# Performance work log

Measured on AMD Instinct MI355X. Metric: run time of the kernel, lower is better.

Reference implementation:

```python
import jax, jax.numpy as jnp
import numpy as np

B, T, L = 512, 512, 128  # batch, seq_len, tag-vocab size (incl. START=126, STOP=127)


def setup_inputs() -> dict:
    key = jax.random.key(0)
    k1, k2, k3 = jax.random.split(key, 3)
    # scale emissions so exp(gold path score) stays finite in fp32
    feats = jax.random.normal(k1, (B, T, L), dtype=jnp.float32) * 0.05
    # xavier_normal on [L, L] -> std = sqrt(2/(L+L)) = 1/sqrt(L)
    transfer = jax.random.normal(k2, (L, L), dtype=jnp.float32) * (1.0 / np.sqrt(L))
    target = jax.random.randint(k3, (B, T), 0, L - 2, dtype=jnp.int32)
    return {"feats": feats, "transfer": transfer, "target": target,
            "start": L - 2, "stop": L - 1}


def _crf_loss(feats, transfer, target, start, stop):
    # feats: [B, T, L] emissions; transfer: [L, L]; target: [B, T] gold tags
    Bb, Tt, Ll = feats.shape

    # ---- forward algorithm (log-sum-exp DP over tags) ----
    # scores[1] = feats[1] + transfer[start, :]
    prev0 = feats[:, 1] + transfer[start][None, :]  # [B, L]

    def step(prev, f_t):
        # original: scores[t, y] = LSE_x( scores[t-1, x] + feats[t, x] + transfer[x, y] )
        v = prev + f_t                                        # [B, L] over prev-tag x
        new = jax.nn.logsumexp(v[:, :, None] + transfer[None, :, :], axis=1)  # [B, L]
        return new, None

    step = jax.checkpoint(step)  # keep scan residuals to just the carries
    feats_rest = jnp.swapaxes(feats[:, 2:], 0, 1)  # [T-2, B, L]
    prev, _ = jax.lax.scan(step, prev0, feats_rest)
    sentence_score = jax.nn.logsumexp(prev + transfer[:, stop][None, :], axis=1)  # [B]

    # ---- gold path score ----
    emit0 = feats[:, 0, start]  # hh[0, start]
    emit = jnp.take_along_axis(feats[:, 1:], target[:, 1:, None], axis=2)[..., 0].sum(axis=1)
    pre = jnp.concatenate(
        [jnp.full((Bb, 1), start, dtype=target.dtype), target[:, 1:Tt - 1]], axis=1)  # [B, T-1]
    # original reads transfer[pre, tgt].data[0] -> detached constant
    trans = jax.lax.stop_gradient(transfer[pre, target[:, 1:]]).sum(axis=1)
    gold_score = jnp.exp(emit0 + emit + trans)  # original returns torch.exp(score)

    return sentence_score - gold_score  # per-sentence loss, shape [B]


def reference(feats, transfer, target, start, stop):
    return _crf_loss(feats, transfer, target, start, stop)
```

## Files before the change

### kernel.cpp

```cpp
#include <hip/hip_runtime.h>
#include <hip/hip_bf16.h>

#define T_DIM 512
#define L_DIM 128

typedef _Float16 h2 __attribute__((ext_vector_type(2)));

#if defined(__has_builtin)
#if __has_builtin(__builtin_amdgcn_fdot2)
#define HAS_FDOT2 1
#endif
#endif

__device__ __forceinline__ float fdot2_acc(h2 a, h2 b, float c) {
#ifdef HAS_FDOT2
    return __builtin_amdgcn_fdot2(a, b, c, false);
#else
    return c + (float)a.x * (float)b.x + (float)a.y * (float)b.y;
#endif
}

__device__ __forceinline__ h2 pack_f16(float a, float b) {
    return __builtin_bit_cast(h2, __builtin_amdgcn_cvt_pkrtz(a, b));
}

__device__ __forceinline__ void lds_barrier() {
    asm volatile("s_waitcnt lgkmcnt(0)\n\ts_barrier" ::: "memory");
}

__global__ __launch_bounds__(512, 4) void crf_fwd_kernel(
    const float* __restrict__ feats,
    const float* __restrict__ transfer,
    const int* __restrict__ target,
    const int* __restrict__ startp,
    const int* __restrict__ stopp,
    float* __restrict__ out)
{
    __shared__ unsigned short LdsU[2][L_DIM] __attribute__((aligned(16)));
    __shared__ float LdsRed[32];

    const int tid  = threadIdx.x;
    const int lane = tid & 63;
    const int wv   = tid >> 6;
    const int jj   = lane & 15;
    const int iq   = lane >> 4;
    const int j    = (wv << 4) | jj;
    const int i0   = iq << 5;
    const int b    = blockIdx.x;
    const int start = startp[0];
    const int stop  = stopp[0];
    const float* fbase = feats + (size_t)b * T_DIM * L_DIM;
    const float LOG128 = 4.852030263919617f;

    h2 Ecol[16];
#pragma unroll
    for (int q = 0; q < 16; ++q) {
        float e0 = __expf(transfer[(i0 + 2 * q)     * L_DIM + j]) * 0.0078125f;
        float e1 = __expf(transfer[(i0 + 2 * q + 1) * L_DIM + j]) * 0.0078125f;
        Ecol[q] = pack_f16(e0, e1);
    }
    const float trStop = transfer[j * L_DIM + stop];

    {
        float v2 = fbase[1 * L_DIM + j] + fbase[2 * L_DIM + j]
                 + transfer[start * L_DIM + j];
        if (iq == 0) {
            _Float16 h = (_Float16)__expf(v2);
            LdsU[0][j] = __builtin_bit_cast(unsigned short, h);
        }
    }
    float fa = fbase[3 * L_DIM + j];
    float fb = fbase[4 * L_DIM + j];
    float S  = 0.f;
    lds_barrier();

    int cur = 0;
    float accFinal = 0.f;

    for (int t = 2; t <= T_DIM - 1; ++t) {
        int tp = t + 3; if (tp > T_DIM - 1) tp = T_DIM - 1;
        float fnew = fbase[tp * L_DIM + j];
        float fexp = __expf(fa);

        if ((t & 15) == 0) {
            _Float16 h0 = __builtin_bit_cast(_Float16, LdsU[cur][0]);
            float u0 = (float)h0;
            fexp *= 1.0f / u0;
            S += __logf(u0);
        }

        const uint4* P4 = reinterpret_cast<const uint4*>(&LdsU[cur][0]);
        uint4 pa = P4[(iq << 2) | 0];
        uint4 pb = P4[(iq << 2) | 1];
        uint4 pc = P4[(iq << 2) | 2];
        uint4 pd = P4[(iq << 2) | 3];

        float a0 = 0.f, a1 = 0.f, a2 = 0.f, a3 = 0.f;
        a0 = fdot2_acc(__builtin_bit_cast(h2, pa.x), Ecol[0],  a0);
        a0 = fdot2_acc(__builtin_bit_cast(h2, pa.y), Ecol[1],  a0);
        a0 = fdot2_acc(__builtin_bit_cast(h2, pa.z), Ecol[2],  a0);
        a0 = fdot2_acc(__builtin_bit_cast(h2, pa.w), Ecol[3],  a0);
        a1 = fdot2_acc(__builtin_bit_cast(h2, pb.x), Ecol[4],  a1);
        a1 = fdot2_acc(__builtin_bit_cast(h2, pb.y), Ecol[5],  a1);
        a1 = fdot2_acc(__builtin_bit_cast(h2, pb.z), Ecol[6],  a1);
        a1 = fdot2_acc(__builtin_bit_cast(h2, pb.w), Ecol[7],  a1);
        a2 = fdot2_acc(__builtin_bit_cast(h2, pc.x), Ecol[8],  a2);
        a2 = fdot2_acc(__builtin_bit_cast(h2, pc.y), Ecol[9],  a2);
        a2 = fdot2_acc(__builtin_bit_cast(h2, pc.z), Ecol[10], a2);
        a2 = fdot2_acc(__builtin_bit_cast(h2, pc.w), Ecol[11], a2);
        a3 = fdot2_acc(__builtin_bit_cast(h2, pd.x), Ecol[12], a3);
        a3 = fdot2_acc(__builtin_bit_cast(h2, pd.y), Ecol[13], a3);
        a3 = fdot2_acc(__builtin_bit_cast(h2, pd.z), Ecol[14], a3);
        a3 = fdot2_acc(__builtin_bit_cast(h2, pd.w), Ecol[15], a3);
        float acc = (a0 + a1) + (a2 + a3);

        acc += __shfl_xor(acc, 16);
        acc += __shfl_xor(acc, 32);

        if (t < T_DIM - 1) {
            float un = acc * fexp;
            fa = fb; fb = fnew;
            if (iq == 0) {
                _Float16 h = (_Float16)un;
                LdsU[cur ^ 1][j] = __builtin_bit_cast(unsigned short, h);
            }
            lds_barrier();
            cur ^= 1;
        } else {
            accFinal = acc;
        }
    }

    S += 510.0f * LOG128;

    float x  = __logf(accFinal) + S + trStop;
    float mx = x;
#pragma unroll
    for (int d = 1; d < 64; d <<= 1) mx = fmaxf(mx, __shfl_xor(mx, d));
    float ex = (iq == 0) ? __expf(x - mx) : 0.f;
#pragma unroll
    for (int d = 1; d < 64; d <<= 1) ex += __shfl_xor(ex, d);
    if (lane == 0) { LdsRed[wv] = mx; LdsRed[8 + wv] = ex; }

    float es = 0.f, ts = 0.f;
    {
        int t = 1 + tid;
        if (t < T_DIM) {
            int tg = target[b * T_DIM + t];
            es = fbase[t * L_DIM + tg];
            int pr = (t == 1) ? start : target[b * T_DIM + t - 1];
            ts = transfer[pr * L_DIM + tg];
        }
    }
#pragma unroll
    for (int d = 1; d < 64; d <<= 1) {
        es += __shfl_xor(es, d);
        ts += __shfl_xor(ts, d);
    }
    if (lane == 0) { LdsRed[16 + wv] = es; LdsRed[24 + wv] = ts; }
    __syncthreads();

    if (tid == 0) {
        float M = LdsRed[0];
#pragma unroll
        for (int k = 1; k < 8; ++k) M = fmaxf(M, LdsRed[k]);
        float Ssum = 0.f;
#pragma unroll
        for (int k = 0; k < 8; ++k) Ssum += LdsRed[8 + k] * __expf(LdsRed[k] - M);
        float sentence = M + __logf(Ssum);
        float em = 0.f, tn = 0.f;
#pragma unroll
        for (int k = 0; k < 8; ++k) { em += LdsRed[16 + k]; tn += LdsRed[24 + k]; }
        float emit0 = fbase[start];
        out[b] = sentence - __expf(emit0 + em + tn);
    }
}

extern "C" void kernel_launch(void* const* d_in, const int* in_sizes, int n_in,
                              void* d_out, int out_size, void* d_ws, size_t ws_size,
                              hipStream_t stream) {
    const float* feats    = (const float*)d_in[0];
    const float* transfer = (const float*)d_in[1];
    const int*   target   = (const int*)d_in[2];
    const int*   startp   = (const int*)d_in[3];
    const int*   stopp    = (const int*)d_in[4];
    float* outp = (float*)d_out;
    int B = in_sizes[0] / (T_DIM * L_DIM);
    hipLaunchKernelGGL(crf_fwd_kernel, dim3(B), dim3(512), 0, stream,
                       feats, transfer, target, startp, stopp, outp);
}
```

Measured before the change: 395.1 us.

## Map each sequence to a single wavefront to eliminate block barriers

Reassigns each sentence's forward recursion to one 64-lane wavefront, with each lane computing two target tags against all 128 previous tags from register-resident exp(transfer) in half precision. Workgroup barriers and cross-lane shuffle reductions per timestep are removed, relying on single-wave execution with only an LDS waitcnt. This trades the serial synchronisation cost for eight times more dot-product work per lane per step and much lower occupancy. Final reductions also collapse to wave-level shuffles.

```diff
diff --git a/kernel.cpp b/kernel.cpp
--- a/kernel.cpp
+++ b/kernel.cpp
@@ -1,10 +1,10 @@
 #include <hip/hip_runtime.h>
-#include <hip/hip_bf16.h>
 
 #define T_DIM 512
 #define L_DIM 128
 
 typedef _Float16 h2 __attribute__((ext_vector_type(2)));
+typedef float f2 __attribute__((ext_vector_type(2)));
 
 #if defined(__has_builtin)
 #if __has_builtin(__builtin_amdgcn_fdot2)
@@ -20,15 +20,15 @@
 #endif
 }
 
-__device__ __forceinline__ h2 pack_f16(float a, float b) {
+__device__ __forceinline__ unsigned int pack_u32(float a, float b) {
+    return __builtin_bit_cast(unsigned int, __builtin_amdgcn_cvt_pkrtz(a, b));
+}
+
+__device__ __forceinline__ h2 pack_h2(float a, float b) {
     return __builtin_bit_cast(h2, __builtin_amdgcn_cvt_pkrtz(a, b));
 }
 
-__device__ __forceinline__ void lds_barrier() {
-    asm volatile("s_waitcnt lgkmcnt(0)\n\ts_barrier" ::: "memory");
-}
-
-__global__ __launch_bounds__(512, 4) void crf_fwd_kernel(
+__global__ __launch_bounds__(64, 1) void crf_fwd_kernel(
     const float* __restrict__ feats,
     const float* __restrict__ transfer,
     const int* __restrict__ target,
@@ -36,120 +36,110 @@
     const int* __restrict__ stopp,
     float* __restrict__ out)
 {
-    __shared__ unsigned short LdsU[2][L_DIM] __attribute__((aligned(16)));
-    __shared__ float LdsRed[32];
+    __shared__ unsigned int LdsU[2][64] __attribute__((aligned(16)));
 
-    const int tid  = threadIdx.x;
-    const int lane = tid & 63;
-    const int wv   = tid >> 6;
-    const int jj   = lane & 15;
-    const int iq   = lane >> 4;
-    const int j    = (wv << 4) | jj;
-    const int i0   = iq << 5;
+    const int lane = threadIdx.x;
+    const int j0   = lane << 1;
     const int b    = blockIdx.x;
     const int start = startp[0];
     const int stop  = stopp[0];
     const float* fbase = feats + (size_t)b * T_DIM * L_DIM;
     const float LOG128 = 4.852030263919617f;
+    const float SCALE  = 0.0078125f;
 
-    h2 Ecol[16];
+    h2 E0[64], E1[64];
 #pragma unroll
-    for (int q = 0; q < 16; ++q) {
-        float e0 = __expf(transfer[(i0 + 2 * q)     * L_DIM + j]) * 0.0078125f;
-        float e1 = __expf(transfer[(i0 + 2 * q + 1) * L_DIM + j]) * 0.0078125f;
-        Ecol[q] = pack_f16(e0, e1);
+    for (int q = 0; q < 64; ++q) {
+        f2 r0 = *reinterpret_cast<const f2*>(&transfer[(2 * q)     * L_DIM + j0]);
+        f2 r1 = *reinterpret_cast<const f2*>(&transfer[(2 * q + 1) * L_DIM + j0]);
+        E0[q] = pack_h2(__expf(r0.x) * SCALE, __expf(r1.x) * SCALE);
+        E1[q] = pack_h2(__expf(r0.y) * SCALE, __expf(r1.y) * SCALE);
     }
-    const float trStop = transfer[j * L_DIM + stop];
+    const float trStop0 = transfer[j0 * L_DIM + stop];
+    const float trStop1 = transfer[(j0 + 1) * L_DIM + stop];
 
     {
-        float v2 = fbase[1 * L_DIM + j] + fbase[2 * L_DIM + j]
-                 + transfer[start * L_DIM + j];
-        if (iq == 0) {
-            _Float16 h = (_Float16)__expf(v2);
-            LdsU[0][j] = __builtin_bit_cast(unsigned short, h);
-        }
+        f2 f1v = *reinterpret_cast<const f2*>(&fbase[1 * L_DIM + j0]);
+        f2 f2v = *reinterpret_cast<const f2*>(&fbase[2 * L_DIM + j0]);
+        f2 tsv = *reinterpret_cast<const f2*>(&transfer[start * L_DIM + j0]);
+        float v0 = f1v.x + f2v.x + tsv.x;
+        float v1 = f1v.y + f2v.y + tsv.y;
+        LdsU[0][lane] = pack_u32(__expf(v0), __expf(v1));
     }
-    float fa = fbase[3 * L_DIM + j];
-    float fb = fbase[4 * L_DIM + j];
-    float S  = 0.f;
-    lds_barrier();
+    f2 fa2 = *reinterpret_cast<const f2*>(&fbase[3 * L_DIM + j0]);
+    f2 fb2 = *reinterpret_cast<const f2*>(&fbase[4 * L_DIM + j0]);
+    f2 fc2 = *reinterpret_cast<const f2*>(&fbase[5 * L_DIM + j0]);
+    float S = 0.f;
+    asm volatile("s_waitcnt lgkmcnt(0)" ::: "memory");
 
     int cur = 0;
-    float accFinal = 0.f;
+    float accF0 = 0.f, accF1 = 0.f;
 
     for (int t = 2; t <= T_DIM - 1; ++t) {
-        int tp = t + 3; if (tp > T_DIM - 1) tp = T_DIM - 1;
-        float fnew = fbase[tp * L_DIM + j];
-        float fexp = __expf(fa);
+        int tp = t + 4; if (tp > T_DIM - 1) tp = T_DIM - 1;
+        f2 fnew2 = *reinterpret_cast<const f2*>(&fbase[tp * L_DIM + j0]);
+        float e0 = __expf(fa2.x);
+        float e1 = __expf(fa2.y);
 
         if ((t & 15) == 0) {
-            _Float16 h0 = __builtin_bit_cast(_Float16, LdsU[cur][0]);
-            float u0 = (float)h0;
-            fexp *= 1.0f / u0;
+            h2 h = __builtin_bit_cast(h2, LdsU[cur][0]);
+            float u0 = (float)h.x;
+            float r = 1.0f / u0;
+            e0 *= r; e1 *= r;
             S += __logf(u0);
         }
 
-        const uint4* P4 = reinterpret_cast<const uint4*>(&LdsU[cur][0]);
-        uint4 pa = P4[(iq << 2) | 0];
-        uint4 pb = P4[(iq << 2) | 1];
-        uint4 pc = P4[(iq << 2) | 2];
-        uint4 pd = P4[(iq << 2) | 3];
-
-        float a0 = 0.f, a1 = 0.f, a2 = 0.f, a3 = 0.f;
-        a0 = fdot2_acc(__builtin_bit_cast(h2, pa.x), Ecol[0],  a0);
-        a0 = fdot2_acc(__builtin_bit_cast(h2, pa.y), Ecol[1],  a0);
-        a0 = fdot2_acc(__builtin_bit_cast(h2, pa.z), Ecol[2],  a0);
-        a0 = fdot2_acc(__builtin_bit_cast(h2, pa.w), Ecol[3],  a0);
-        a1 = fdot2_acc(__builtin_bit_cast(h2, pb.x), Ecol[4],  a1);
-        a1 = fdot2_acc(__builtin_bit_cast(h2, pb.y), Ecol[5],  a1);
-        a1 = fdot2_acc(__builtin_bit_cast(h2, pb.z), Ecol[6],  a1);
-        a1 = fdot2_acc(__builtin_bit_cast(h2, pb.w), Ecol[7],  a1);
-        a2 = fdot2_acc(__builtin_bit_cast(h2, pc.x), Ecol[8],  a2);
-        a2 = fdot2_acc(__builtin_bit_cast(h2, pc.y), Ecol[9],  a2);
-        a2 = fdot2_acc(__builtin_bit_cast(h2, pc.z), Ecol[10], a2);
-        a2 = fdot2_acc(__builtin_bit_cast(h2, pc.w), Ecol[11], a2);
-        a3 = fdot2_acc(__builtin_bit_cast(h2, pd.x), Ecol[12], a3);
-        a3 = fdot2_acc(__builtin_bit_cast(h2, pd.y), Ecol[13], a3);
-        a3 = fdot2_acc(__builtin_bit_cast(h2, pd.z), Ecol[14], a3);
-        a3 = fdot2_acc(__builtin_bit_cast(h2, pd.w), Ecol[15], a3);
-        float acc = (a0 + a1) + (a2 + a3);
-
-        acc += __shfl_xor(acc, 16);
-        acc += __shfl_xor(acc, 32);
+        const uint4* U4 = reinterpret_cast<const uint4*>(&LdsU[cur][0]);
+        float a0[4] = {0.f, 0.f, 0.f, 0.f};
+        float a1[4] = {0.f, 0.f, 0.f, 0.f};
+#pragma unroll
+        for (int g = 0; g < 16; ++g) {
+            uint4 p = U4[g];
+            const int c = g >> 2;
+            a0[c] = fdot2_acc(__builtin_bit_cast(h2, p.x), E0[4 * g + 0], a0[c]);
+            a0[c] = fdot2_acc(__builtin_bit_cast(h2, p.y), E0[4 * g + 1], a0[c]);
+            a0[c] = fdot2_acc(__builtin_bit_cast(h2, p.z), E0[4 * g + 2], a0[c]);
+            a0[c] = fdot2_acc(__builtin_bit_cast(h2, p.w), E0[4 * g + 3], a0[c]);
+            a1[c] = fdot2_acc(__builtin_bit_cast(h2, p.x), E1[4 * g + 0], a1[c]);
+            a1[c] = fdot2_acc(__builtin_bit_cast(h2, p.y), E1[4 * g + 1], a1[c]);
+            a1[c] = fdot2_acc(__builtin_bit_cast(h2, p.z), E1[4 * g + 2], a1[c]);
+            a1[c] = fdot2_acc(__builtin_bit_cast(h2, p.w), E1[4 * g + 3], a1[c]);
+        }
+        float acc0 = (a0[0] + a0[1]) + (a0[2] + a0[3]);
+        float acc1 = (a1[0] + a1[1]) + (a1[2] + a1[3]);
 
         if (t < T_DIM - 1) {
-            float un = acc * fexp;
-            fa = fb; fb = fnew;
-            if (iq == 0) {
-                _Float16 h = (_Float16)un;
-                LdsU[cur ^ 1][j] = __builtin_bit_cast(unsigned short, h);
-            }
-            lds_barrier();
+            LdsU[cur ^ 1][lane] = pack_u32(acc0 * e0, acc1 * e1);
+            asm volatile("s_waitcnt lgkmcnt(0)" ::: "memory");
             cur ^= 1;
+            fa2 = fb2; fb2 = fc2; fc2 = fnew2;
         } else {
-            accFinal = acc;
+            accF0 = acc0; accF1 = acc1;
         }
     }
 
     S += 510.0f * LOG128;
 
-    float x  = __logf(accFinal) + S + trStop;
-    float mx = x;
+    float x0 = __logf(accF0) + S + trStop0;
+    float x1 = __logf(accF1) + S + trStop1;
+    float mx = fmaxf(x0, x1);
 #pragma unroll
     for (int d = 1; d < 64; d <<= 1) mx = fmaxf(mx, __shfl_xor(mx, d));
-    float ex = (iq == 0) ? __expf(x - mx) : 0.f;
+    float ex = __expf(x0 - mx) + __expf(x1 - mx);
 #pragma unroll
     for (int d = 1; d < 64; d <<= 1) ex += __shfl_xor(ex, d);
-    if (lane == 0) { LdsRed[wv] = mx; LdsRed[8 + wv] = ex; }
+    float sentence = mx + __logf(ex);
 
     float es = 0.f, ts = 0.f;
-    {
-        int t = 1 + tid;
+    const int* tgt = target + b * T_DIM;
+#pragma unroll
+    for (int k = 0; k < 8; ++k) {
+        int t = 1 + lane + (k << 6);
         if (t < T_DIM) {
-            int tg = target[b * T_DIM + t];
-            es = fbase[t * L_DIM + tg];
-            int pr = (t == 1) ? start : target[b * T_DIM + t - 1];
-            ts = transfer[pr * L_DIM + tg];
+            int tg = tgt[t];
+            es += fbase[t * L_DIM + tg];
+            int pr = (t == 1) ? start : tgt[t - 1];
+            ts += transfer[pr * L_DIM + tg];
         }
     }
 #pragma unroll
@@ -157,22 +147,9 @@
         es += __shfl_xor(es, d);
         ts += __shfl_xor(ts, d);
     }
-    if (lane == 0) { LdsRed[16 + wv] = es; LdsRed[24 + wv] = ts; }
-    __syncthreads();
-
-    if (tid == 0) {
-        float M = LdsRed[0];
-#pragma unroll
-        for (int k = 1; k < 8; ++k) M = fmaxf(M, LdsRed[k]);
-        float Ssum = 0.f;
-#pragma unroll
-        for (int k = 0; k < 8; ++k) Ssum += LdsRed[8 + k] * __expf(LdsRed[k] - M);
-        float sentence = M + __logf(Ssum);
-        float em = 0.f, tn = 0.f;
-#pragma unroll
-        for (int k = 0; k < 8; ++k) { em += LdsRed[16 + k]; tn += LdsRed[24 + k]; }
+    if (lane == 0) {
         float emit0 = fbase[start];
-        out[b] = sentence - __expf(emit0 + em + tn);
+        out[b] = sentence - __expf(emit0 + es + ts);
     }
 }
 
@@ -186,6 +163,6 @@
     const int*   stopp    = (const int*)d_in[4];
     float* outp = (float*)d_out;
     int B = in_sizes[0] / (T_DIM * L_DIM);
-    hipLaunchKernelGGL(crf_fwd_kernel, dim3(B), dim3(512), 0, stream,
+    hipLaunchKernelGGL(crf_fwd_kernel, dim3(B), dim3(64), 0, stream,
                        feats, transfer, target, startp, stopp, outp);
 }
```

After: 419.3 us. 6.1% more time.
